# Performance work log

Hardware: AMD Instinct MI355X
Metric: run time of the kernel (lower is better)

The kernel has to match this reference:

```python
import jax, jax.numpy as jnp
import numpy as np

B, T, S, C, HS = 4, 4096, 4096, 1024, 64

def setup_inputs() -> dict:
    key = jax.random.key(0)
    k1, k2, k3, k4, k5 = jax.random.split(key, 5)
    x = jax.random.normal(k1, (B, T, C), dtype=jnp.float32)
    encode_out = jax.random.normal(k2, (B, S, C), dtype=jnp.float32)
    # nn.Linear(C, HS, bias=False): weight [HS, C]; store transposed [C, HS] for x @ W
    sc = 1.0 / np.sqrt(C)
    Wk = jax.random.uniform(k3, (C, HS), dtype=jnp.float32, minval=-sc, maxval=sc)
    Wq = jax.random.uniform(k4, (C, HS), dtype=jnp.float32, minval=-sc, maxval=sc)
    Wv = jax.random.uniform(k5, (C, HS), dtype=jnp.float32, minval=-sc, maxval=sc)
    return {"x": x, "encode_out": encode_out, "Wq": Wq, "Wk": Wk, "Wv": Wv}

def reference(x, encode_out, Wq, Wk, Wv):
    # Single-head cross-attention (mask=False path)
    q = x @ Wq                      # [B, T, HS]
    k = encode_out @ Wk             # [B, S, HS]
    v = encode_out @ Wv             # [B, S, HS]
    scale = k.shape[-1] ** -0.5
    wei = jnp.einsum('btd,bsd->bts', q, k) * scale   # [B, T, S]
    wei = jax.nn.softmax(wei, axis=-1)
    out = jnp.einsum('bts,bsd->btd', wei, v)         # [B, T, HS]
    return out
```

## Files before the change

### kernel.cpp

```cpp
#include <hip/hip_runtime.h>
#include <hip/hip_bf16.h>

#define TT 4096
#define SS 4096
#define CC 1024
#define HS 64

typedef __bf16 bf16x8 __attribute__((ext_vector_type(8)));
typedef __bf16 bf16x4 __attribute__((ext_vector_type(4)));
typedef float  f32x4  __attribute__((ext_vector_type(4)));
typedef float  f32x16 __attribute__((ext_vector_type(16)));

#define MFMA16(A,B,C) __builtin_amdgcn_mfma_f32_16x16x32_bf16((A),(B),(C),0,0,0)
#define MFMA32(A,B,C) __builtin_amdgcn_mfma_f32_32x32x16_bf16((A),(B),(C),0,0,0)

__device__ __forceinline__ int pkbf(float a, float b) {
    union { struct { __bf16 lo, hi; } h; int i; } u;
    u.h.lo = (__bf16)a; u.h.hi = (__bf16)b;
    return u.i;
}

__device__ __forceinline__ bf16x8 cvt8(float4 f0, float4 f1) {
    bf16x8 a;
    a[0] = (__bf16)f0.x; a[1] = (__bf16)f0.y; a[2] = (__bf16)f0.z; a[3] = (__bf16)f0.w;
    a[4] = (__bf16)f1.x; a[5] = (__bf16)f1.y; a[6] = (__bf16)f1.z; a[7] = (__bf16)f1.w;
    return a;
}

__device__ __forceinline__ void gload_lds16(const void* g, char* l) {
    __builtin_amdgcn_global_load_lds(
        (const __attribute__((address_space(1))) void*)g,
        (__attribute__((address_space(3))) void*)l, 16, 0, 0);
}

__global__ __launch_bounds__(256) void prep_wt(const float* __restrict__ Wq,
                                               const float* __restrict__ Wk,
                                               const float* __restrict__ Wv,
                                               __bf16* __restrict__ wt) {
    int idx = blockIdx.x * 256 + threadIdx.x;
    int mat = idx >> 16;
    int e   = idx & 65535;
    int d   = e >> 10;
    int kk  = e & 1023;
    const float* W = (mat == 0) ? Wq : (mat == 1 ? Wk : Wv);
    float v = W[kk * HS + d];
    if (mat == 0) v *= 0.125f * 1.44269504088896340736f;
    wt[idx] = (__bf16)v;
}

__global__ __launch_bounds__(512, 1) void proj_qkv(const float* __restrict__ x,
                                                   const float* __restrict__ enc,
                                                   const __bf16* __restrict__ wt,
                                                   __bf16* __restrict__ qb,
                                                   __bf16* __restrict__ kb,
                                                   __bf16* __restrict__ vt) {
    extern __shared__ char smem[];
    int tid = threadIdx.x;
    int w = tid >> 6, l = tid & 63, lq = l >> 4, lm = l & 15;
    int kv   = blockIdx.x & 1;
    int row0 = (blockIdx.x >> 1) * 128;
    int rowbase = row0 + w * 16;
    const float*  src   = kv ? enc : x;
    const __bf16* wbase = wt + (kv ? HS * CC : 0);
    const __bf16* wvb   = wt + 2 * HS * CC;

    #define STAGE_A(k) do {                                                             \
        _Pragma("unroll")                                                               \
        for (int j = 0; j < 4; ++j) {                                                   \
            int rloc = j * 4 + (l >> 4);                                                \
            int gs = (l & 15) ^ rloc;                                                   \
            gload_lds16(src + (size_t)(rowbase + rloc) * CC + (k) * 64 + gs * 4,        \
                        smem + ((k) % 3) * 32768 + w * 4096 + j * 1024);                \
        }                                                                               \
    } while (0)

    #define STAGE_B(k, mptr, moff) do {                                                 \
        int gs = (l & 7) ^ (l >> 3);                                                    \
        gload_lds16(mptr + (size_t)(w * 8 + (l >> 3)) * CC + (k) * 64 + gs * 8,         \
                    smem + 98304 + ((k) & 1) * 16384 + (moff) + w * 1024);              \
    } while (0)

    f32x4 accA[4], accV[4];
    #pragma unroll
    for (int i = 0; i < 4; i++) { accA[i] = (f32x4){0.f,0.f,0.f,0.f}; accV[i] = (f32x4){0.f,0.f,0.f,0.f}; }

    if (kv) {
        STAGE_B(0, wbase, 0); STAGE_B(0, wvb, 8192);
        STAGE_A(0); STAGE_A(1);
        #pragma unroll
        for (int k = 0; k < 16; ++k) {
            if (k < 15) { STAGE_B(k + 1, wbase, 0); STAGE_B(k + 1, wvb, 8192); }
            if (k < 14) STAGE_A(k + 2);
            if (k < 14)      asm volatile("s_waitcnt vmcnt(10)\ns_barrier" ::: "memory");
            else if (k == 14) asm volatile("s_waitcnt vmcnt(6)\ns_barrier" ::: "memory");
            else              asm volatile("s_waitcnt vmcnt(0)\ns_barrier" ::: "memory");

            const char* Ab = smem + (k % 3) * 32768 + w * 4096;
            const char* Bb = smem + 98304 + (k & 1) * 16384;
            #pragma unroll
            for (int ks = 0; ks < 2; ++ks) {
                int g0 = ks * 8 + lq * 2;
                float4 f0 = *(const float4*)(Ab + lm * 256 + ((g0)     ^ lm) * 16);
                float4 f1 = *(const float4*)(Ab + lm * 256 + ((g0 + 1) ^ lm) * 16);
                bf16x8 af = cvt8(f0, f1);
                int bg = ((ks * 4 + lq) ^ (lm & 7)) * 16;
                #pragma unroll
                for (int nt = 0; nt < 4; nt++) {
                    bf16x8 bA = *(const bf16x8*)(Bb + (nt * 16 + lm) * 128 + bg);
                    bf16x8 bV = *(const bf16x8*)(Bb + 8192 + (nt * 16 + lm) * 128 + bg);
                    accA[nt] = MFMA16(af, bA, accA[nt]);
                    accV[nt] = MFMA16(af, bV, accV[nt]);
                }
            }
            asm volatile("s_waitcnt lgkmcnt(0)\ns_barrier" ::: "memory");
        }
    } else {
        STAGE_B(0, wbase, 0);
        STAGE_A(0); STAGE_A(1);
        #pragma unroll
        for (int k = 0; k < 16; ++k) {
            if (k < 15) STAGE_B(k + 1, wbase, 0);
            if (k < 14) STAGE_A(k + 2);
            if (k < 14)      asm volatile("s_waitcnt vmcnt(9)\ns_barrier" ::: "memory");
            else if (k == 14) asm volatile("s_waitcnt vmcnt(5)\ns_barrier" ::: "memory");
            else              asm volatile("s_waitcnt vmcnt(0)\ns_barrier" ::: "memory");

            const char* Ab = smem + (k % 3) * 32768 + w * 4096;
            const char* Bb = smem + 98304 + (k & 1) * 16384;
            #pragma unroll
            for (int ks = 0; ks < 2; ++ks) {
                int g0 = ks * 8 + lq * 2;
                float4 f0 = *(const float4*)(Ab + lm * 256 + ((g0)     ^ lm) * 16);
                float4 f1 = *(const float4*)(Ab + lm * 256 + ((g0 + 1) ^ lm) * 16);
                bf16x8 af = cvt8(f0, f1);
                int bg = ((ks * 4 + lq) ^ (lm & 7)) * 16;
                #pragma unroll
                for (int nt = 0; nt < 4; nt++) {
                    bf16x8 bA = *(const bf16x8*)(Bb + (nt * 16 + lm) * 128 + bg);
                    accA[nt] = MFMA16(af, bA, accA[nt]);
                }
            }
            asm volatile("s_waitcnt lgkmcnt(0)\ns_barrier" ::: "memory");
        }
    }
    #undef STAGE_A
    #undef STAGE_B

    {
        __bf16* dstA = kv ? kb : qb;
        #pragma unroll
        for (int nt = 0; nt < 4; nt++)
            #pragma unroll
            for (int r = 0; r < 4; r++)
                dstA[(size_t)(rowbase + lq * 4 + r) * HS + nt * 16 + lm] = (__bf16)accA[nt][r];
    }
    if (kv) {
        int bb = row0 >> 12;
        int sbase = (row0 & 4095) + w * 16 + lq * 4;
        #pragma unroll
        for (int nt = 0; nt < 4; nt++) {
            bf16x4 pk = { (__bf16)accV[nt][0], (__bf16)accV[nt][1],
                          (__bf16)accV[nt][2], (__bf16)accV[nt][3] };
            *(bf16x4*)(vt + ((size_t)bb * HS + nt * 16 + lm) * SS + sbase) = pk;
        }
    }
}

__global__ __launch_bounds__(512, 1) void attn(const __bf16* __restrict__ qb,
                                               const __bf16* __restrict__ kb,
                                               const __bf16* __restrict__ vt,
                                               float* __restrict__ out) {
    extern __shared__ char smem[];
    int tid = threadIdx.x, w = tid >> 6, l = tid & 63;
    int hi = l >> 5, ln = l & 31;
    int qg = w & 1, ss = w >> 1;

    int bid = blockIdx.x;
    int b = bid & 3, tb = bid >> 2;
    int t0 = tb * 64;

    const __bf16* qp = qb + ((size_t)(b * TT + t0 + qg * 32 + ln)) * HS + hi * 8;
    bf16x8 qf[4];
    qf[0] = *(const bf16x8*)(qp);
    qf[1] = *(const bf16x8*)(qp + 16);
    qf[2] = *(const bf16x8*)(qp + 32);
    qf[3] = *(const bf16x8*)(qp + 48);

    const __bf16* kbase = kb + (size_t)b * SS * HS;
    const __bf16* vbase = vt + (size_t)b * HS * SS;

    #define STAGE(t, p) do {                                                            \
        _Pragma("unroll")                                                               \
        for (int i = 0; i < 4; ++i) {                                                   \
            int idx = i * 512 + tid;                                                    \
            int sr = idx >> 3, g = idx & 7;                                             \
            gload_lds16(kbase + ((size_t)(t) * 256 + sr) * 64 + ((g ^ (sr & 7)) * 8),   \
                        smem + (p) * 65536 + idx * 16);                                 \
        }                                                                               \
        _Pragma("unroll")                                                               \
        for (int i = 0; i < 4; ++i) {                                                   \
            int idx = i * 512 + tid;                                                    \
            int dr = idx >> 5, g = idx & 31;                                            \
            gload_lds16(vbase + (size_t)dr * SS + (t) * 256 + ((g ^ (dr & 7)) * 8),     \
                        smem + (p) * 65536 + 32768 + idx * 16);                         \
        }                                                                               \
    } while (0)

    f32x16 oacc0, oacc1;
    #pragma unroll
    for (int i = 0; i < 16; i++) { oacc0[i] = 0.f; oacc1[i] = 0.f; }
    float lsum = 0.f;

    STAGE(0, 0);
    for (int t = 0; t < 16; ++t) {
        int p = t & 1;
        if (t < 15) {
            STAGE(t + 1, p ^ 1);
            asm volatile("s_waitcnt vmcnt(8)\ns_barrier" ::: "memory");
        } else {
            asm volatile("s_waitcnt vmcnt(0)\ns_barrier" ::: "memory");
        }
        const char* Kb = smem + p * 65536;
        const char* Vb = smem + p * 65536 + 32768;

        #pragma unroll
        for (int sg = 0; sg < 2; ++sg) {
            int srow = ss * 64 + sg * 32 + ln;
            bf16x8 ka[4];
            #pragma unroll
            for (int ks = 0; ks < 4; ++ks)
                ka[ks] = *(const bf16x8*)(Kb + srow * 128 + (((ks * 2 + hi) ^ (srow & 7)) * 16));

            f32x16 s;
            #pragma unroll
            for (int i = 0; i < 16; i++) s[i] = 0.f;
            s = MFMA32(ka[0], qf[0], s);
            s = MFMA32(ka[1], qf[1], s);
            s = MFMA32(ka[2], qf[2], s);
            s = MFMA32(ka[3], qf[3], s);

            float pv[16];
            #pragma unroll
            for (int i = 0; i < 16; i++) pv[i] = __builtin_amdgcn_exp2f(s[i]);
            float l0 = (pv[0] + pv[1]) + (pv[2] + pv[3]);
            float l1 = (pv[4] + pv[5]) + (pv[6] + pv[7]);
            float l2 = (pv[8] + pv[9]) + (pv[10] + pv[11]);
            float l3 = (pv[12] + pv[13]) + (pv[14] + pv[15]);
            lsum += (l0 + l1) + (l2 + l3);

            int d01 = pkbf(pv[0],  pv[1]),  d23 = pkbf(pv[2],  pv[3]);
            int d45 = pkbf(pv[4],  pv[5]),  d67 = pkbf(pv[6],  pv[7]);
            int e01 = pkbf(pv[8],  pv[9]),  e23 = pkbf(pv[10], pv[11]);
            int e45 = pkbf(pv[12], pv[13]), e67 = pkbf(pv[14], pv[15]);
            asm("v_permlane32_swap_b32 %0, %1" : "+v"(d01), "+v"(d45));
            asm("v_permlane32_swap_b32 %0, %1" : "+v"(d23), "+v"(d67));
            asm("v_permlane32_swap_b32 %0, %1" : "+v"(e01), "+v"(e45));
            asm("v_permlane32_swap_b32 %0, %1" : "+v"(e23), "+v"(e67));
            union F { int i[4]; bf16x8 v; } f0, f1;
            f0.i[0] = d01; f0.i[1] = d23; f0.i[2] = d45; f0.i[3] = d67;
            f1.i[0] = e01; f1.i[1] = e23; f1.i[2] = e45; f1.i[3] = e67;

            int ksp = ss * 4 + sg * 2;
            #pragma unroll
            for (int dg = 0; dg < 2; ++dg) {
                int d = dg * 32 + ln;
                bf16x8 va0 = *(const bf16x8*)(Vb + d * 512 + ((((ksp)     * 2 + hi) ^ (d & 7)) * 16));
                bf16x8 va1 = *(const bf16x8*)(Vb + d * 512 + ((((ksp + 1) * 2 + hi) ^ (d & 7)) * 16));
                if (dg == 0) { oacc0 = MFMA32(va0, f0.v, oacc0); oacc0 = MFMA32(va1, f1.v, oacc0); }
                else         { oacc1 = MFMA32(va0, f0.v, oacc1); oacc1 = MFMA32(va1, f1.v, oacc1); }
            }
        }
        asm volatile("s_waitcnt lgkmcnt(0)\ns_barrier" ::: "memory");
    }
    #undef STAGE

    lsum += __shfl_xor(lsum, 32, 64);

    float* accC = (float*)smem;
    float* lsC  = (float*)(smem + 102400);
    union O { f32x16 v; f32x4 q[4]; } o0, o1;
    o0.v = oacc0; o1.v = oacc1;
    {
        int b0 = ((qg * 4 + ss) * 2 + 0) * 1280 + l * 20;
        int b1 = ((qg * 4 + ss) * 2 + 1) * 1280 + l * 20;
        #pragma unroll
        for (int g = 0; g < 4; ++g) {
            *(f32x4*)&accC[b0 + g * 4] = o0.q[g];
            *(f32x4*)&accC[b1 + g * 4] = o1.q[g];
        }
        if (l < 32) lsC[(qg * 4 + ss) * 32 + l] = lsum;
    }
    __syncthreads();

    {
        int q = tid >> 3, c8 = tid & 7;
        int qg2 = q >> 5, ln2 = q & 31;
        float ls = 0.f;
        #pragma unroll
        for (int s2 = 0; s2 < 4; ++s2) ls += lsC[(qg2 * 4 + s2) * 32 + ln2];
        float inv = 1.0f / ls;
        float vout[8];
        #pragma unroll
        for (int j = 0; j < 8; ++j) {
            int d = c8 * 8 + j;
            int hi2 = (d >> 2) & 1, dg = d >> 5;
            int r = (((d & 31) >> 3) << 2) | (d & 3);
            float sum = 0.f;
            #pragma unroll
            for (int s2 = 0; s2 < 4; ++s2)
                sum += accC[((qg2 * 4 + s2) * 2 + dg) * 1280 + (hi2 * 32 + ln2) * 20 + r];
            vout[j] = sum * inv;
        }
        float* orow = out + (size_t)(b * TT + t0 + q) * HS + c8 * 8;
        *(f32x4*)(orow)     = *(f32x4*)&vout[0];
        *(f32x4*)(orow + 4) = *(f32x4*)&vout[4];
    }
}

extern "C" void kernel_launch(void* const* d_in, const int* in_sizes, int n_in,
                              void* d_out, int out_size, void* d_ws, size_t ws_size,
                              hipStream_t stream) {
    (void)in_sizes; (void)n_in; (void)out_size; (void)ws_size;
    const float* x   = (const float*)d_in[0];
    const float* enc = (const float*)d_in[1];
    const float* Wq  = (const float*)d_in[2];
    const float* Wk  = (const float*)d_in[3];
    const float* Wv  = (const float*)d_in[4];
    float* out = (float*)d_out;

    char* ws = (char*)d_ws;
    __bf16* wtb  = (__bf16*)ws;
    __bf16* qbuf = (__bf16*)(ws + 393216);
    __bf16* kbuf = (__bf16*)(ws + 393216 + 2097152);
    __bf16* vbuf = (__bf16*)(ws + 393216 + 2 * 2097152);

    hipLaunchKernelGGL(prep_wt,  dim3(768), dim3(256), 0,      stream, Wq, Wk, Wv, wtb);
    hipLaunchKernelGGL(proj_qkv, dim3(256), dim3(512), 131072, stream, x, enc, wtb, qbuf, kbuf, vbuf);
    hipLaunchKernelGGL(attn,     dim3(256), dim3(512), 131072, stream, qbuf, kbuf, vbuf, out);
}
```

Measured before the change: 65.12 us.

## Split projection K-dimension across warp pairs and double grid size

The projection kernel now processes 64 rows per block instead of 128, with the two halves of the C dimension split across warp pairs and reduced through shared memory at the end. Weight tiles are read straight from global memory into registers rather than staged in LDS, the activation buffer drops from triple to double buffering with no per-step barriers, and LDS use falls to 64KB so more blocks can fit per CU. This is meant to raise parallelism and occupancy in the memory-bound projection. The cost is redundant global weight loads per wave and an extra shared-memory reduction step.

```diff
diff --git a/kernel.cpp b/kernel.cpp
--- a/kernel.cpp
+++ b/kernel.cpp
@@ -48,7 +48,7 @@
     wt[idx] = (__bf16)v;
 }
 
-__global__ __launch_bounds__(512, 1) void proj_qkv(const float* __restrict__ x,
+__global__ __launch_bounds__(512, 4) void proj_qkv(const float* __restrict__ x,
                                                    const float* __restrict__ enc,
                                                    const __bf16* __restrict__ wt,
                                                    __bf16* __restrict__ qb,
@@ -57,111 +57,133 @@
     extern __shared__ char smem[];
     int tid = threadIdx.x;
     int w = tid >> 6, l = tid & 63, lq = l >> 4, lm = l & 15;
+    int rg = w >> 1, kh = w & 1;
     int kv   = blockIdx.x & 1;
-    int row0 = (blockIdx.x >> 1) * 128;
-    int rowbase = row0 + w * 16;
-    const float*  src   = kv ? enc : x;
-    const __bf16* wbase = wt + (kv ? HS * CC : 0);
-    const __bf16* wvb   = wt + 2 * HS * CC;
-
-    #define STAGE_A(k) do {                                                             \
+    int row0 = (blockIdx.x >> 1) * 64;
+    int rowbase = row0 + rg * 16;
+    int kbase0  = kh * 512;
+    const float*  src = kv ? enc : x;
+    const __bf16* wA  = wt + (kv ? HS * CC : 0);
+    const __bf16* wV  = wt + 2 * HS * CC;
+
+    #define STAGE_A(s) do {                                                             \
         _Pragma("unroll")                                                               \
         for (int j = 0; j < 4; ++j) {                                                   \
             int rloc = j * 4 + (l >> 4);                                                \
             int gs = (l & 15) ^ rloc;                                                   \
-            gload_lds16(src + (size_t)(rowbase + rloc) * CC + (k) * 64 + gs * 4,        \
-                        smem + ((k) % 3) * 32768 + w * 4096 + j * 1024);                \
+            gload_lds16(src + (size_t)(rowbase + rloc) * CC + kbase0 + (s) * 64 + gs * 4, \
+                        smem + ((s) & 1) * 32768 + w * 4096 + j * 1024);                \
         }                                                                               \
-    } while (0)
-
-    #define STAGE_B(k, mptr, moff) do {                                                 \
-        int gs = (l & 7) ^ (l >> 3);                                                    \
-        gload_lds16(mptr + (size_t)(w * 8 + (l >> 3)) * CC + (k) * 64 + gs * 8,         \
-                    smem + 98304 + ((k) & 1) * 16384 + (moff) + w * 1024);              \
     } while (0)
 
     f32x4 accA[4], accV[4];
     #pragma unroll
     for (int i = 0; i < 4; i++) { accA[i] = (f32x4){0.f,0.f,0.f,0.f}; accV[i] = (f32x4){0.f,0.f,0.f,0.f}; }
 
+    STAGE_A(0);
+
     if (kv) {
-        STAGE_B(0, wbase, 0); STAGE_B(0, wvb, 8192);
-        STAGE_A(0); STAGE_A(1);
-        #pragma unroll
-        for (int k = 0; k < 16; ++k) {
-            if (k < 15) { STAGE_B(k + 1, wbase, 0); STAGE_B(k + 1, wvb, 8192); }
-            if (k < 14) STAGE_A(k + 2);
-            if (k < 14)      asm volatile("s_waitcnt vmcnt(10)\ns_barrier" ::: "memory");
-            else if (k == 14) asm volatile("s_waitcnt vmcnt(6)\ns_barrier" ::: "memory");
-            else              asm volatile("s_waitcnt vmcnt(0)\ns_barrier" ::: "memory");
-
-            const char* Ab = smem + (k % 3) * 32768 + w * 4096;
-            const char* Bb = smem + 98304 + (k & 1) * 16384;
+        #pragma unroll
+        for (int s = 0; s < 8; ++s) {
+            bf16x8 bA[2][4], bV[2][4];
+            #pragma unroll
+            for (int nt = 0; nt < 4; nt++) {
+                const __bf16* pa = wA + (size_t)(nt * 16 + lm) * CC + kbase0 + s * 64 + lq * 8;
+                const __bf16* pv = wV + (size_t)(nt * 16 + lm) * CC + kbase0 + s * 64 + lq * 8;
+                bA[0][nt] = *(const bf16x8*)(pa);
+                bA[1][nt] = *(const bf16x8*)(pa + 32);
+                bV[0][nt] = *(const bf16x8*)(pv);
+                bV[1][nt] = *(const bf16x8*)(pv + 32);
+            }
+            if (s < 7) {
+                STAGE_A(s + 1);
+                asm volatile("s_waitcnt vmcnt(20)" ::: "memory");
+            } else {
+                asm volatile("s_waitcnt vmcnt(16)" ::: "memory");
+            }
+            const char* Ab = smem + (s & 1) * 32768 + w * 4096;
             #pragma unroll
             for (int ks = 0; ks < 2; ++ks) {
                 int g0 = ks * 8 + lq * 2;
                 float4 f0 = *(const float4*)(Ab + lm * 256 + ((g0)     ^ lm) * 16);
                 float4 f1 = *(const float4*)(Ab + lm * 256 + ((g0 + 1) ^ lm) * 16);
                 bf16x8 af = cvt8(f0, f1);
-                int bg = ((ks * 4 + lq) ^ (lm & 7)) * 16;
                 #pragma unroll
                 for (int nt = 0; nt < 4; nt++) {
-                    bf16x8 bA = *(const bf16x8*)(Bb + (nt * 16 + lm) * 128 + bg);
-                    bf16x8 bV = *(const bf16x8*)(Bb + 8192 + (nt * 16 + lm) * 128 + bg);
-                    accA[nt] = MFMA16(af, bA, accA[nt]);
-                    accV[nt] = MFMA16(af, bV, accV[nt]);
+                    accA[nt] = MFMA16(af, bA[ks][nt], accA[nt]);
+                    accV[nt] = MFMA16(af, bV[ks][nt], accV[nt]);
                 }
             }
-            asm volatile("s_waitcnt lgkmcnt(0)\ns_barrier" ::: "memory");
         }
     } else {
-        STAGE_B(0, wbase, 0);
-        STAGE_A(0); STAGE_A(1);
-        #pragma unroll
-        for (int k = 0; k < 16; ++k) {
-            if (k < 15) STAGE_B(k + 1, wbase, 0);
-            if (k < 14) STAGE_A(k + 2);
-            if (k < 14)      asm volatile("s_waitcnt vmcnt(9)\ns_barrier" ::: "memory");
-            else if (k == 14) asm volatile("s_waitcnt vmcnt(5)\ns_barrier" ::: "memory");
-            else              asm volatile("s_waitcnt vmcnt(0)\ns_barrier" ::: "memory");
-
-            const char* Ab = smem + (k % 3) * 32768 + w * 4096;
-            const char* Bb = smem + 98304 + (k & 1) * 16384;
+        #pragma unroll
+        for (int s = 0; s < 8; ++s) {
+            bf16x8 bA[2][4];
+            #pragma unroll
+            for (int nt = 0; nt < 4; nt++) {
+                const __bf16* pa = wA + (size_t)(nt * 16 + lm) * CC + kbase0 + s * 64 + lq * 8;
+                bA[0][nt] = *(const bf16x8*)(pa);
+                bA[1][nt] = *(const bf16x8*)(pa + 32);
+            }
+            if (s < 7) {
+                STAGE_A(s + 1);
+                asm volatile("s_waitcnt vmcnt(12)" ::: "memory");
+            } else {
+                asm volatile("s_waitcnt vmcnt(8)" ::: "memory");
+            }
+            const char* Ab = smem + (s & 1) * 32768 + w * 4096;
             #pragma unroll
             for (int ks = 0; ks < 2; ++ks) {
                 int g0 = ks * 8 + lq * 2;
                 float4 f0 = *(const float4*)(Ab + lm * 256 + ((g0)     ^ lm) * 16);
                 float4 f1 = *(const float4*)(Ab + lm * 256 + ((g0 + 1) ^ lm) * 16);
                 bf16x8 af = cvt8(f0, f1);
-                int bg = ((ks * 4 + lq) ^ (lm & 7)) * 16;
                 #pragma unroll
-                for (int nt = 0; nt < 4; nt++) {
-                    bf16x8 bA = *(const bf16x8*)(Bb + (nt * 16 + lm) * 128 + bg);
-                    accA[nt] = MFMA16(af, bA, accA[nt]);
-                }
-            }
-            asm volatile("s_waitcnt lgkmcnt(0)\ns_barrier" ::: "memory");
+                for (int nt = 0; nt < 4; nt++)
+                    accA[nt] = MFMA16(af, bA[ks][nt], accA[nt]);
+            }
         }
     }
     #undef STAGE_A
-    #undef STAGE_B
-
-    {
+
+    __syncthreads();
+    if (kh == 1) {
+        char* dump = smem + rg * 8192;
+        #pragma unroll
+        for (int g = 0; g < 4; ++g)
+            *(f32x4*)(dump + (g * 64 + l) * 16) = accA[g];
+        if (kv) {
+            #pragma unroll
+            for (int g = 0; g < 4; ++g)
+                *(f32x4*)(dump + ((4 + g) * 64 + l) * 16) = accV[g];
+        }
+    }
+    __syncthreads();
+    if (kh == 0) {
+        const char* dump = smem + rg * 8192;
+        #pragma unroll
+        for (int g = 0; g < 4; ++g)
+            accA[g] += *(const f32x4*)(dump + (g * 64 + l) * 16);
+        if (kv) {
+            #pragma unroll
+            for (int g = 0; g < 4; ++g)
+                accV[g] += *(const f32x4*)(dump + ((4 + g) * 64 + l) * 16);
+        }
         __bf16* dstA = kv ? kb : qb;
         #pragma unroll
         for (int nt = 0; nt < 4; nt++)
             #pragma unroll
             for (int r = 0; r < 4; r++)
                 dstA[(size_t)(rowbase + lq * 4 + r) * HS + nt * 16 + lm] = (__bf16)accA[nt][r];
-    }
-    if (kv) {
-        int bb = row0 >> 12;
-        int sbase = (row0 & 4095) + w * 16 + lq * 4;
-        #pragma unroll
-        for (int nt = 0; nt < 4; nt++) {
-            bf16x4 pk = { (__bf16)accV[nt][0], (__bf16)accV[nt][1],
-                          (__bf16)accV[nt][2], (__bf16)accV[nt][3] };
-            *(bf16x4*)(vt + ((size_t)bb * HS + nt * 16 + lm) * SS + sbase) = pk;
+        if (kv) {
+            int bb = row0 >> 12;
+            int sbase = (row0 & 4095) + rg * 16 + lq * 4;
+            #pragma unroll
+            for (int nt = 0; nt < 4; nt++) {
+                bf16x4 pk = { (__bf16)accV[nt][0], (__bf16)accV[nt][1],
+                              (__bf16)accV[nt][2], (__bf16)accV[nt][3] };
+                *(bf16x4*)(vt + ((size_t)bb * HS + nt * 16 + lm) * SS + sbase) = pk;
+            }
         }
     }
 }
@@ -335,6 +357,6 @@
     __bf16* vbuf = (__bf16*)(ws + 393216 + 2 * 2097152);
 
     hipLaunchKernelGGL(prep_wt,  dim3(768), dim3(256), 0,      stream, Wq, Wk, Wv, wtb);
-    hipLaunchKernelGGL(proj_qkv, dim3(256), dim3(512), 131072, stream, x, enc, wtb, qbuf, kbuf, vbuf);
+    hipLaunchKernelGGL(proj_qkv, dim3(512), dim3(512), 65536,  stream, x, enc, wtb, qbuf, kbuf, vbuf);
     hipLaunchKernelGGL(attn,     dim3(256), dim3(512), 131072, stream, qbuf, kbuf, vbuf, out);
 }
```

Result: slower. 109.8 us (+68.6%).

## Keep projection weights in registers and stream full-K input row strips

Applied to the files above, without the earlier changes.

The QKV projection kernel now has each wave hold its 16-column slice of the weight matrix (all of K) in registers. It streams 16-row strips of the fp32 input, each spanning the full 1024 columns, through double-buffered LDS, in place of tiling over K with weights staged through LDS. Each wave computes one 16x16 output tile per strip, and launch bounds ask for two blocks per CU. This removes repeated weight traffic through LDS and the per-K-step barriers, at the cost of 128 registers of B fragments and idle waves in Q blocks, where only four of eight waves compute. The 128KB LDS footprint may also block the requested two-block occupancy.

```diff
diff --git a/kernel.cpp b/kernel.cpp
--- a/kernel.cpp
+++ b/kernel.cpp
@@ -48,7 +48,7 @@
     wt[idx] = (__bf16)v;
 }
 
-__global__ __launch_bounds__(512, 1) void proj_qkv(const float* __restrict__ x,
+__global__ __launch_bounds__(512, 2) void proj_qkv(const float* __restrict__ x,
                                                    const float* __restrict__ enc,
                                                    const __bf16* __restrict__ wt,
                                                    __bf16* __restrict__ qb,
@@ -59,111 +59,71 @@
     int w = tid >> 6, l = tid & 63, lq = l >> 4, lm = l & 15;
     int kv   = blockIdx.x & 1;
     int row0 = (blockIdx.x >> 1) * 128;
-    int rowbase = row0 + w * 16;
-    const float*  src   = kv ? enc : x;
-    const __bf16* wbase = wt + (kv ? HS * CC : 0);
-    const __bf16* wvb   = wt + 2 * HS * CC;
-
-    #define STAGE_A(k) do {                                                             \
+    const float* src = kv ? enc : x;
+
+    int  cg   = w & 3;
+    bool comp = kv ? true : (w < 4);
+    int  mat  = kv ? ((w < 4) ? 1 : 2) : 0;
+
+    bf16x8 B[32];
+    if (comp) {
+        const __bf16* bp = wt + (size_t)mat * HS * CC + (size_t)(cg * 16 + lm) * CC + lq * 8;
+        #pragma unroll
+        for (int ks = 0; ks < 32; ++ks)
+            B[ks] = *(const bf16x8*)(bp + ks * 32);
+    }
+
+    #define STAGE(g) do {                                                               \
         _Pragma("unroll")                                                               \
-        for (int j = 0; j < 4; ++j) {                                                   \
-            int rloc = j * 4 + (l >> 4);                                                \
-            int gs = (l & 15) ^ rloc;                                                   \
-            gload_lds16(src + (size_t)(rowbase + rloc) * CC + (k) * 64 + gs * 4,        \
-                        smem + ((k) % 3) * 32768 + w * 4096 + j * 1024);                \
+        for (int ii = 0; ii < 8; ++ii) {                                                \
+            int i  = w * 8 + ii;                                                        \
+            int r  = i >> 2;                                                            \
+            int q4 = i & 3;                                                             \
+            int gl = q4 * 64 + l;                                                       \
+            int gs = (gl & ~15) | ((gl ^ r) & 15);                                      \
+            gload_lds16(src + (size_t)(row0 + (g) * 16 + r) * CC + gs * 4,              \
+                        smem + ((g) & 1) * 65536 + r * 4096 + q4 * 1024);               \
         }                                                                               \
     } while (0)
 
-    #define STAGE_B(k, mptr, moff) do {                                                 \
-        int gs = (l & 7) ^ (l >> 3);                                                    \
-        gload_lds16(mptr + (size_t)(w * 8 + (l >> 3)) * CC + (k) * 64 + gs * 8,         \
-                    smem + 98304 + ((k) & 1) * 16384 + (moff) + w * 1024);              \
-    } while (0)
-
-    f32x4 accA[4], accV[4];
+    STAGE(0);
     #pragma unroll
-    for (int i = 0; i < 4; i++) { accA[i] = (f32x4){0.f,0.f,0.f,0.f}; accV[i] = (f32x4){0.f,0.f,0.f,0.f}; }
-
-    if (kv) {
-        STAGE_B(0, wbase, 0); STAGE_B(0, wvb, 8192);
-        STAGE_A(0); STAGE_A(1);
-        #pragma unroll
-        for (int k = 0; k < 16; ++k) {
-            if (k < 15) { STAGE_B(k + 1, wbase, 0); STAGE_B(k + 1, wvb, 8192); }
-            if (k < 14) STAGE_A(k + 2);
-            if (k < 14)      asm volatile("s_waitcnt vmcnt(10)\ns_barrier" ::: "memory");
-            else if (k == 14) asm volatile("s_waitcnt vmcnt(6)\ns_barrier" ::: "memory");
-            else              asm volatile("s_waitcnt vmcnt(0)\ns_barrier" ::: "memory");
-
-            const char* Ab = smem + (k % 3) * 32768 + w * 4096;
-            const char* Bb = smem + 98304 + (k & 1) * 16384;
-            #pragma unroll
-            for (int ks = 0; ks < 2; ++ks) {
+    for (int p = 0; p < 8; ++p) {
+        if (p < 7) {
+            STAGE(p + 1);
+            asm volatile("s_waitcnt vmcnt(8)\ns_barrier" ::: "memory");
+        } else {
+            asm volatile("s_waitcnt vmcnt(0)\ns_barrier" ::: "memory");
+        }
+        if (comp) {
+            const char* Ab = smem + (p & 1) * 65536 + (size_t)lm * 4096;
+            f32x4 acc = (f32x4){0.f, 0.f, 0.f, 0.f};
+            #pragma unroll
+            for (int ks = 0; ks < 32; ++ks) {
                 int g0 = ks * 8 + lq * 2;
-                float4 f0 = *(const float4*)(Ab + lm * 256 + ((g0)     ^ lm) * 16);
-                float4 f1 = *(const float4*)(Ab + lm * 256 + ((g0 + 1) ^ lm) * 16);
-                bf16x8 af = cvt8(f0, f1);
-                int bg = ((ks * 4 + lq) ^ (lm & 7)) * 16;
+                int b0 = (g0 & ~15) | ((g0 ^ lm) & 15);
+                int g1 = g0 + 1;
+                int b1 = (g1 & ~15) | ((g1 ^ lm) & 15);
+                float4 f0 = *(const float4*)(Ab + b0 * 16);
+                float4 f1 = *(const float4*)(Ab + b1 * 16);
+                acc = MFMA16(cvt8(f0, f1), B[ks], acc);
+            }
+            int grow = row0 + p * 16;
+            if (mat < 2) {
+                __bf16* dst = kv ? kb : qb;
                 #pragma unroll
-                for (int nt = 0; nt < 4; nt++) {
-                    bf16x8 bA = *(const bf16x8*)(Bb + (nt * 16 + lm) * 128 + bg);
-                    bf16x8 bV = *(const bf16x8*)(Bb + 8192 + (nt * 16 + lm) * 128 + bg);
-                    accA[nt] = MFMA16(af, bA, accA[nt]);
-                    accV[nt] = MFMA16(af, bV, accV[nt]);
-                }
+                for (int r = 0; r < 4; ++r)
+                    dst[(size_t)(grow + lq * 4 + r) * HS + cg * 16 + lm] = (__bf16)acc[r];
+            } else {
+                int bb = row0 >> 12;
+                int sb = (grow & 4095) + lq * 4;
+                bf16x4 pk = { (__bf16)acc[0], (__bf16)acc[1], (__bf16)acc[2], (__bf16)acc[3] };
+                *(bf16x4*)(vt + ((size_t)bb * HS + cg * 16 + lm) * SS + sb) = pk;
             }
-            asm volatile("s_waitcnt lgkmcnt(0)\ns_barrier" ::: "memory");
-        }
-    } else {
-        STAGE_B(0, wbase, 0);
-        STAGE_A(0); STAGE_A(1);
-        #pragma unroll
-        for (int k = 0; k < 16; ++k) {
-            if (k < 15) STAGE_B(k + 1, wbase, 0);
-            if (k < 14) STAGE_A(k + 2);
-            if (k < 14)      asm volatile("s_waitcnt vmcnt(9)\ns_barrier" ::: "memory");
-            else if (k == 14) asm volatile("s_waitcnt vmcnt(5)\ns_barrier" ::: "memory");
-            else              asm volatile("s_waitcnt vmcnt(0)\ns_barrier" ::: "memory");
-
-            const char* Ab = smem + (k % 3) * 32768 + w * 4096;
-            const char* Bb = smem + 98304 + (k & 1) * 16384;
-            #pragma unroll
-            for (int ks = 0; ks < 2; ++ks) {
-                int g0 = ks * 8 + lq * 2;
-                float4 f0 = *(const float4*)(Ab + lm * 256 + ((g0)     ^ lm) * 16);
-                float4 f1 = *(const float4*)(Ab + lm * 256 + ((g0 + 1) ^ lm) * 16);
-                bf16x8 af = cvt8(f0, f1);
-                int bg = ((ks * 4 + lq) ^ (lm & 7)) * 16;
-                #pragma unroll
-                for (int nt = 0; nt < 4; nt++) {
-                    bf16x8 bA = *(const bf16x8*)(Bb + (nt * 16 + lm) * 128 + bg);
-                    accA[nt] = MFMA16(af, bA, accA[nt]);
-                }
-            }
-            asm volatile("s_waitcnt lgkmcnt(0)\ns_barrier" ::: "memory");
-        }
-    }
-    #undef STAGE_A
-    #undef STAGE_B
-
-    {
-        __bf16* dstA = kv ? kb : qb;
-        #pragma unroll
-        for (int nt = 0; nt < 4; nt++)
-            #pragma unroll
-            for (int r = 0; r < 4; r++)
-                dstA[(size_t)(rowbase + lq * 4 + r) * HS + nt * 16 + lm] = (__bf16)accA[nt][r];
-    }
-    if (kv) {
-        int bb = row0 >> 12;
-        int sbase = (row0 & 4095) + w * 16 + lq * 4;
-        #pragma unroll
-        for (int nt = 0; nt < 4; nt++) {
-            bf16x4 pk = { (__bf16)accV[nt][0], (__bf16)accV[nt][1],
-                          (__bf16)accV[nt][2], (__bf16)accV[nt][3] };
-            *(bf16x4*)(vt + ((size_t)bb * HS + nt * 16 + lm) * SS + sbase) = pk;
-        }
-    }
+        }
+        asm volatile("s_waitcnt lgkmcnt(0)\ns_barrier" ::: "memory");
+    }
+    #undef STAGE
 }
 
 __global__ __launch_bounds__(512, 1) void attn(const __bf16* __restrict__ qb,
```

Result: slower. 72.03 us (+10.6%).
